# Kernel optimization log

Hardware: AMD Instinct MI355X
Metric: run time of the kernel (lower is better)

Reference implementation:

```python
import jax, jax.numpy as jnp
import numpy as np

DIM = 256
HEADS = 8
H = 56
W = 56
WS = 7          # window size
SHIFT = 3       # cyclic shift
MLP_HIDDEN = 4 * DIM
HEAD_DIM = DIM // HEADS
SCALE = HEAD_DIM ** -0.5
N = WS * WS     # tokens per window
EPS = 1e-5


def _rel_pos_index():
    coords = np.stack(np.meshgrid(np.arange(WS), np.arange(WS), indexing='ij'))  # [2,ws,ws]
    cf = coords.reshape(2, -1)                       # [2, N]
    rel = cf[:, :, None] - cf[:, None, :]            # [2, N, N]
    rel = rel.transpose(1, 2, 0).copy()              # [N, N, 2]
    rel[:, :, 0] += WS - 1
    rel[:, :, 1] += WS - 1
    rel[:, :, 1] *= 2 * WS - 1
    return rel.sum(-1)                               # [N, N]

REL_IDX = jnp.asarray(_rel_pos_index())


def _attn_mask():
    # shifted-window attention mask, computed once (static)
    img = np.zeros((H, W))
    cnt = 0
    slices = (slice(0, -WS), slice(-WS, -SHIFT), slice(-SHIFT, None))
    for hs in slices:
        for ws in slices:
            img[hs, ws] = cnt
            cnt += 1
    mw = img.reshape(H // WS, WS, W // WS, WS).transpose(0, 2, 1, 3).reshape(-1, N)  # [nW, N]
    am = mw[:, None, :] - mw[:, :, None]
    return jnp.asarray(np.where(am != 0, -100.0, 0.0).astype(np.float32))  # [nW, N, N]

ATTN_MASK = _attn_mask()


def _layernorm(y, g, b):
    mu = y.mean(-1, keepdims=True)
    var = ((y - mu) ** 2).mean(-1, keepdims=True)
    return (y - mu) * jax.lax.rsqrt(var + EPS) * g + b


def setup_inputs() -> dict:
    key = jax.random.key(0)
    ks = jax.random.split(key, 10)
    B = 32
    x = jax.random.normal(ks[0], (B, H * W, DIM), dtype=jnp.float32)
    qkv_w = jax.random.normal(ks[1], (DIM, 3 * DIM), dtype=jnp.float32) * 0.02
    qkv_b = jnp.zeros((3 * DIM,), dtype=jnp.float32)
    proj_w = jax.random.normal(ks[2], (DIM, DIM), dtype=jnp.float32) * 0.02
    proj_b = jnp.zeros((DIM,), dtype=jnp.float32)
    bias_table = jax.random.normal(ks[3], ((2 * WS - 1) * (2 * WS - 1), HEADS), dtype=jnp.float32) * 0.02
    norm1_g = jnp.ones((DIM,), dtype=jnp.float32)
    norm1_b = jnp.zeros((DIM,), dtype=jnp.float32)
    norm2_g = jnp.ones((DIM,), dtype=jnp.float32)
    norm2_b = jnp.zeros((DIM,), dtype=jnp.float32)
    mlp_w1 = jax.random.normal(ks[4], (DIM, MLP_HIDDEN), dtype=jnp.float32) * 0.02
    mlp_b1 = jnp.zeros((MLP_HIDDEN,), dtype=jnp.float32)
    mlp_w2 = jax.random.normal(ks[5], (MLP_HIDDEN, DIM), dtype=jnp.float32) * 0.02
    mlp_b2 = jnp.zeros((DIM,), dtype=jnp.float32)
    return dict(x=x, norm1_g=norm1_g, norm1_b=norm1_b, qkv_w=qkv_w, qkv_b=qkv_b,
                proj_w=proj_w, proj_b=proj_b, bias_table=bias_table,
                norm2_g=norm2_g, norm2_b=norm2_b,
                mlp_w1=mlp_w1, mlp_b1=mlp_b1, mlp_w2=mlp_w2, mlp_b2=mlp_b2)


def reference(x, norm1_g, norm1_b, qkv_w, qkv_b, proj_w, proj_b, bias_table,
              norm2_g, norm2_b, mlp_w1, mlp_b1, mlp_w2, mlp_b2):
    B, M, C = x.shape
    shortcut = x
    y = _layernorm(x, norm1_g, norm1_b).reshape(B, H, W, C)
    # cyclic shift
    y = jnp.roll(y, (-SHIFT, -SHIFT), axis=(1, 2))
    # window partition: [B,H,W,C] -> [B*nW, N, C]
    win = y.reshape(B, H // WS, WS, W // WS, WS, C).transpose(0, 1, 3, 2, 4, 5).reshape(-1, N, C)
    Bw = win.shape[0]
    qkv = (win @ qkv_w + qkv_b).reshape(Bw, N, 3, HEADS, HEAD_DIM).transpose(2, 0, 3, 1, 4)
    q, k, v = qkv[0], qkv[1], qkv[2]               # each [Bw, heads, N, hd]
    attn = jnp.einsum('bhnd,bhmd->bhnm', q, k) * SCALE
    bias = bias_table[REL_IDX].transpose(2, 0, 1)  # [heads, N, N]
    attn = attn + bias[None]
    nW = ATTN_MASK.shape[0]
    attn = attn.reshape(B, nW, HEADS, N, N) + ATTN_MASK[None, :, None]
    attn = jax.nn.softmax(attn.reshape(Bw, HEADS, N, N), axis=-1)
    out = jnp.einsum('bhnm,bhmd->bhnd', attn, v).transpose(0, 2, 1, 3).reshape(Bw, N, C)
    out = out @ proj_w + proj_b
    # window reverse and un-shift
    out = out.reshape(B, H // WS, W // WS, WS, WS, C).transpose(0, 1, 3, 2, 4, 5).reshape(B, H, W, C)
    out = jnp.roll(out, (SHIFT, SHIFT), axis=(1, 2)).reshape(B, M, C)
    x = shortcut + out
    h = _layernorm(x, norm2_g, norm2_b)
    h = jax.nn.gelu(h @ mlp_w1 + mlp_b1) @ mlp_w2 + mlp_b2
    return x + h
```

## Files before the change

### kernel.cpp

```cpp
#include <hip/hip_runtime.h>
#include <hip/hip_bf16.h>
#include <math.h>

typedef __bf16 bf16_t;
typedef __attribute__((ext_vector_type(8))) __bf16 bf16x8;
typedef __attribute__((ext_vector_type(4))) __bf16 bf16x4;
typedef __attribute__((ext_vector_type(4))) float f32x4;

#define T_TOK 100352
#define DIMC 256
#define HEADS 8
#define HD 32
#define NTOK 49
#define SHIFT3 3
#define HH 56
#define SCALE_QK 0.17677669529663687f

__device__ __forceinline__ int xrow_of(int rr) {
    int wi = rr / 49; int t = rr - wi * 49;
    int b = wi >> 6; int w64 = wi & 63;
    int wh = w64 >> 3, ww = w64 & 7;
    int i = t / 7, j = t - i * 7;
    int hy = wh * 7 + i, wy = ww * 7 + j;
    int hx = hy + SHIFT3; if (hx >= HH) hx -= HH;
    int wx = wy + SHIFT3; if (wx >= HH) wx -= HH;
    return b * (HH * HH) + hx * HH + wx;
}

__global__ __launch_bounds__(256) void transpose_cast(const float* __restrict__ W,
                                                      bf16_t* __restrict__ WT,
                                                      int K, int Nc) {
    int t = blockIdx.x * 256 + threadIdx.x;
    int k = t / Nc, c = t - k * Nc;
    WT[(size_t)c * K + k] = (bf16_t)W[t];
}

template <int MAP>
__global__ __launch_bounds__(256) void ln_kernel(const float* __restrict__ x,
                                                 const float* __restrict__ g,
                                                 const float* __restrict__ bsh,
                                                 bf16_t* __restrict__ out) {
    int wv = threadIdx.x >> 6, l = threadIdx.x & 63;
    int r = blockIdx.x * 4 + wv;
    int xr = MAP ? xrow_of(r) : r;
    float4 v = ((const float4*)(x + (size_t)xr * DIMC))[l];
    float s = v.x + v.y + v.z + v.w;
    float sq = v.x * v.x + v.y * v.y + v.z * v.z + v.w * v.w;
    #pragma unroll
    for (int off = 32; off; off >>= 1) {
        s += __shfl_down(s, off);
        sq += __shfl_down(sq, off);
    }
    s = __shfl(s, 0); sq = __shfl(sq, 0);
    float mean = s * (1.f / 256.f);
    float var = sq * (1.f / 256.f) - mean * mean;
    float rstd = rsqrtf(var + 1e-5f);
    float4 gv = ((const float4*)g)[l];
    float4 bv = ((const float4*)bsh)[l];
    bf16x4 o;
    o[0] = (bf16_t)((v.x - mean) * rstd * gv.x + bv.x);
    o[1] = (bf16_t)((v.y - mean) * rstd * gv.y + bv.y);
    o[2] = (bf16_t)((v.z - mean) * rstd * gv.z + bv.z);
    o[3] = (bf16_t)((v.w - mean) * rstd * gv.w + bv.w);
    *(bf16x4*)(out + (size_t)r * DIMC + l * 4) = o;
}

template <int EPI>
__global__ __launch_bounds__(256) void gemm128(const bf16_t* __restrict__ A,
                                               const bf16_t* __restrict__ BT,
                                               const float* __restrict__ bias,
                                               int Nc, int K,
                                               bf16_t* __restrict__ outb,
                                               float* __restrict__ outf,
                                               const float* __restrict__ resid) {
    __shared__ bf16_t As[128 * 32];
    __shared__ bf16_t Bs[128 * 32];
    int tid = threadIdx.x;
    int wv = tid >> 6, l = tid & 63;
    int wr = wv >> 1, wc = wv & 1;
    int nTilesN = Nc >> 7;
    int bm = blockIdx.x / nTilesN, bn = blockIdx.x - bm * nTilesN;
    size_t row0 = (size_t)bm * 128;
    int col0 = bn * 128;

    const char* Abase = (const char*)(A + row0 * K);
    const char* Bbase = (const char*)(BT + (size_t)col0 * K);
    const size_t ldb = (size_t)K * 2;

    f32x4 acc[4][4] = {};
    const int lr = l & 15, lk = (l >> 4) * 8;
    const int aoff = (wr * 64 + lr) * 32 + lk;
    const int boff = (wc * 64 + lr) * 32 + lk;

    for (int kk = 0; kk < K; kk += 32) {
        #pragma unroll
        for (int it = 0; it < 2; ++it) {
            int t = tid + it * 256;
            int row = t >> 2, cb = (t & 3) * 16;
            __builtin_amdgcn_global_load_lds(
                (const __attribute__((address_space(1))) void*)(Abase + (size_t)row * ldb + (size_t)kk * 2 + cb),
                (__attribute__((address_space(3))) void*)((char*)As + t * 16), 16, 0, 0);
            __builtin_amdgcn_global_load_lds(
                (const __attribute__((address_space(1))) void*)(Bbase + (size_t)row * ldb + (size_t)kk * 2 + cb),
                (__attribute__((address_space(3))) void*)((char*)Bs + t * 16), 16, 0, 0);
        }
        __syncthreads();
        bf16x8 a[4], b[4];
        #pragma unroll
        for (int m = 0; m < 4; ++m) a[m] = *(const bf16x8*)(As + aoff + m * 16 * 32);
        #pragma unroll
        for (int n = 0; n < 4; ++n) b[n] = *(const bf16x8*)(Bs + boff + n * 16 * 32);
        #pragma unroll
        for (int m = 0; m < 4; ++m)
            #pragma unroll
            for (int n = 0; n < 4; ++n)
                acc[m][n] = __builtin_amdgcn_mfma_f32_16x16x32_bf16(a[m], b[n], acc[m][n], 0, 0, 0);
        __syncthreads();
    }

    #pragma unroll
    for (int m = 0; m < 4; ++m) {
        #pragma unroll
        for (int i = 0; i < 4; ++i) {
            int rr = (int)row0 + wr * 64 + m * 16 + (l >> 4) * 4 + i;
            size_t orow = (EPI == 3) ? (size_t)xrow_of(rr) * DIMC : (size_t)rr * Nc;
            #pragma unroll
            for (int n = 0; n < 4; ++n) {
                int cc = col0 + wc * 64 + n * 16 + (l & 15);
                float v = acc[m][n][i] + bias[cc];
                if (EPI == 0) {
                    outb[(size_t)rr * Nc + cc] = (bf16_t)v;
                } else if (EPI == 1) {
                    float t = v + 0.044715f * v * v * v;
                    float gl = 0.5f * v * (1.f + tanhf(0.7978845608028654f * t));
                    outb[(size_t)rr * Nc + cc] = (bf16_t)gl;
                } else if (EPI == 2) {
                    size_t o = (size_t)rr * Nc + cc;
                    outf[o] = v + resid[o];
                } else {
                    size_t o = orow + cc;
                    outf[o] = v + resid[o];
                }
            }
        }
    }
}

__global__ __launch_bounds__(256) void attn_mfma(const bf16_t* __restrict__ qkv,
                                                 const float* __restrict__ bt,
                                                 bf16_t* __restrict__ out) {
    __shared__ __align__(16) char lds[4][12800];
    int wv = threadIdx.x >> 6, l = threadIdx.x & 63;
    int head = ((blockIdx.x & 1) << 2) | wv;
    int wi = blockIdx.x >> 1;
    char* W = lds[wv];
    bf16_t* Vt = (bf16_t*)(W + 8192);
    size_t rowbase = (size_t)wi * NTOK;
    const bf16_t* src = qkv + rowbase * 768 + head * HD;

    int w64 = wi & 63;
    int wh = w64 >> 3, ww = w64 & 7;
    bool lastH = (wh == 7), lastW = (ww == 7);
    bool masked = lastH || lastW;

    #pragma unroll
    for (int it = 0; it < 4; ++it) {
        int t = l + it * 64;
        int r = t >> 2, g = t & 3;
        if (r < NTOK) {
            bf16x8 qv = *(const bf16x8*)(src + (size_t)r * 768 + g * 8);
            bf16x8 kv = *(const bf16x8*)(src + (size_t)r * 768 + 256 + g * 8);
            int sa = (r * 64 + g * 16) ^ ((r & 7) << 4);
            *(bf16x8*)(W + sa) = qv;
            *(bf16x8*)(W + 4096 + sa) = kv;
        }
    }
    #pragma unroll
    for (int it = 0; it < 4; ++it) {
        int t = l + it * 64;
        int m = t >> 2, dc = t & 3;
        if (m < NTOK) {
            bf16x8 vv = *(const bf16x8*)(src + (size_t)m * 768 + 512 + dc * 8);
            #pragma unroll
            for (int j = 0; j < 8; ++j) Vt[(dc * 8 + j) * 72 + m] = vv[j];
        } else {
            #pragma unroll
            for (int j = 0; j < 8; ++j) Vt[(dc * 8 + j) * 72 + m] = (bf16_t)0.f;
        }
    }

    int lr = l & 15, g4 = l >> 4;

    bf16x8 a[4], b[4];
    #pragma unroll
    for (int mt = 0; mt < 4; ++mt) {
        int r = mt * 16 + lr;
        int sa = (r * 64 + g4 * 16) ^ ((r & 7) << 4);
        a[mt] = *(const bf16x8*)(W + sa);
        b[mt] = *(const bf16x8*)(W + 4096 + sa);
    }
    f32x4 z = {0.f, 0.f, 0.f, 0.f};
    f32x4 S[4][4];
    #pragma unroll
    for (int mt = 0; mt < 4; ++mt)
        #pragma unroll
        for (int nt = 0; nt < 4; ++nt)
            S[mt][nt] = __builtin_amdgcn_mfma_f32_16x16x32_bf16(a[mt], b[nt], z, 0, 0, 0);

    int i2[4], j2[4], reg2[4];
    #pragma unroll
    for (int nt = 0; nt < 4; ++nt) {
        int cm = nt * 16 + lr;
        i2[nt] = (cm * 147) >> 10;
        j2[nt] = cm - i2[nt] * 7;
        int rh = lastH ? ((i2[nt] < 4) ? 1 : 2) : 0;
        int rw = lastW ? ((j2[nt] < 4) ? 1 : 2) : 0;
        reg2[nt] = rh * 3 + rw;
    }

    #pragma unroll
    for (int mt = 0; mt < 4; ++mt) {
        #pragma unroll
        for (int i = 0; i < 4; ++i) {
            int rn = mt * 16 + g4 * 4 + i;
            bool rowok = rn < NTOK;
            int i1 = (rn * 147) >> 10, j1 = rn - i1 * 7;
            int rh1 = lastH ? ((i1 < 4) ? 1 : 2) : 0;
            int rw1 = lastW ? ((j1 < 4) ? 1 : 2) : 0;
            int reg1 = rh1 * 3 + rw1;
            float sv[4];
            #pragma unroll
            for (int nt = 0; nt < 4; ++nt) {
                int cm = nt * 16 + lr;
                float s;
                if (rowok && cm < NTOK) {
                    s = S[mt][nt][i] * SCALE_QK;
                    s += bt[((i1 - i2[nt] + 6) + 13 * (j1 - j2[nt] + 6)) * 8 + head];
                    if (masked && (reg1 != reg2[nt])) s -= 100.f;
                } else {
                    s = -1e30f;
                }
                sv[nt] = s;
            }
            float mx = fmaxf(fmaxf(sv[0], sv[1]), fmaxf(sv[2], sv[3]));
            mx = fmaxf(mx, __shfl_xor(mx, 1));
            mx = fmaxf(mx, __shfl_xor(mx, 2));
            mx = fmaxf(mx, __shfl_xor(mx, 4));
            mx = fmaxf(mx, __shfl_xor(mx, 8));
            float e[4];
            float sum = 0.f;
            #pragma unroll
            for (int nt = 0; nt < 4; ++nt) { e[nt] = __expf(sv[nt] - mx); sum += e[nt]; }
            sum += __shfl_xor(sum, 1);
            sum += __shfl_xor(sum, 2);
            sum += __shfl_xor(sum, 4);
            sum += __shfl_xor(sum, 8);
            float inv = 1.f / sum;
            #pragma unroll
            for (int nt = 0; nt < 4; ++nt) {
                int cm = nt * 16 + lr;
                int pa = (rn * 128 + cm * 2) ^ ((rn & 7) << 4);
                *(bf16_t*)(W + pa) = (bf16_t)(e[nt] * inv);
            }
        }
    }

    f32x4 o[4][2] = {};
    #pragma unroll
    for (int ks = 0; ks < 2; ++ks) {
        bf16x8 pa[4], vb[2];
        #pragma unroll
        for (int mt = 0; mt < 4; ++mt) {
            int r = mt * 16 + lr;
            int ad = (r * 128 + ks * 64 + g4 * 16) ^ ((r & 7) << 4);
            pa[mt] = *(const bf16x8*)(W + ad);
        }
        #pragma unroll
        for (int dt = 0; dt < 2; ++dt) {
            int d = dt * 16 + lr;
            vb[dt] = *(const bf16x8*)((char*)Vt + d * 144 + ks * 64 + g4 * 16);
        }
        #pragma unroll
        for (int mt = 0; mt < 4; ++mt)
            #pragma unroll
            for (int dt = 0; dt < 2; ++dt)
                o[mt][dt] = __builtin_amdgcn_mfma_f32_16x16x32_bf16(pa[mt], vb[dt], o[mt][dt], 0, 0, 0);
    }

    #pragma unroll
    for (int mt = 0; mt < 4; ++mt) {
        #pragma unroll
        for (int i = 0; i < 4; ++i) {
            int n = mt * 16 + g4 * 4 + i;
            if (n < NTOK) {
                #pragma unroll
                for (int dt = 0; dt < 2; ++dt) {
                    out[(rowbase + n) * DIMC + head * HD + dt * 16 + lr] = (bf16_t)o[mt][dt][i];
                }
            }
        }
    }
}

extern "C" void kernel_launch(void* const* d_in, const int* in_sizes, int n_in,
                              void* d_out, int out_size, void* d_ws, size_t ws_size,
                              hipStream_t stream) {
    const float* x      = (const float*)d_in[0];
    const float* n1g    = (const float*)d_in[1];
    const float* n1b    = (const float*)d_in[2];
    const float* qkv_w  = (const float*)d_in[3];
    const float* qkv_b  = (const float*)d_in[4];
    const float* proj_w = (const float*)d_in[5];
    const float* proj_b = (const float*)d_in[6];
    const float* btab   = (const float*)d_in[7];
    const float* n2g    = (const float*)d_in[8];
    const float* n2b    = (const float*)d_in[9];
    const float* w1     = (const float*)d_in[10];
    const float* b1     = (const float*)d_in[11];
    const float* w2     = (const float*)d_in[12];
    const float* b2     = (const float*)d_in[13];

    char* ws = (char*)d_ws;
    bf16_t* win      = (bf16_t*)(ws);
    bf16_t* qkvbuf   = (bf16_t*)(ws + (size_t)T_TOK * 256 * 2);
    bf16_t* mlp1_buf = (bf16_t*)(ws);
    bf16_t* h2       = (bf16_t*)(ws + (size_t)T_TOK * 2048);
    char* wtp        = ws + (size_t)T_TOK * 2048 + (size_t)T_TOK * 512;
    bf16_t* wt_qkv   = (bf16_t*)wtp;
    bf16_t* wt_proj  = wt_qkv + 768 * 256;
    bf16_t* wt_mlp1  = wt_proj + 256 * 256;
    bf16_t* wt_mlp2  = wt_mlp1 + 1024 * 256;
    float* xmid      = (float*)d_out;

    transpose_cast<<<768, 256, 0, stream>>>(qkv_w, wt_qkv, 256, 768);
    transpose_cast<<<256, 256, 0, stream>>>(proj_w, wt_proj, 256, 256);
    transpose_cast<<<1024, 256, 0, stream>>>(w1, wt_mlp1, 256, 1024);
    transpose_cast<<<1024, 256, 0, stream>>>(w2, wt_mlp2, 1024, 256);

    ln_kernel<1><<<T_TOK / 4, 256, 0, stream>>>(x, n1g, n1b, win);
    gemm128<0><<<(T_TOK / 128) * (768 / 128), 256, 0, stream>>>(win, wt_qkv, qkv_b, 768, 256,
                                                                qkvbuf, nullptr, nullptr);
    attn_mfma<<<2048 * 2, 256, 0, stream>>>(qkvbuf, btab, win);
    gemm128<3><<<(T_TOK / 128) * (256 / 128), 256, 0, stream>>>(win, wt_proj, proj_b, 256, 256,
                                                                nullptr, xmid, x);
    ln_kernel<0><<<T_TOK / 4, 256, 0, stream>>>(xmid, n2g, n2b, h2);
    gemm128<1><<<(T_TOK / 128) * (1024 / 128), 256, 0, stream>>>(h2, wt_mlp1, b1, 1024, 256,
                                                                 mlp1_buf, nullptr, nullptr);
    gemm128<2><<<(T_TOK / 128) * (256 / 128), 256, 0, stream>>>(mlp1_buf, wt_mlp2, b2, 256, 1024,
                                                                nullptr, xmid, xmid);
}
```

Baseline: 599.6 us.

## Fuse LayerNorm2, MLP fc1+GELU and fc2 into one kernel; remap GEMM blocks

Replaces the second LayerNorm, the fc1 GEMM with GELU epilogue and the fc2 GEMM with one kernel. Each 64-row block normalises its rows in registers, streams 128-column slices of W1 into LDS, writes the GELU output to swizzled LDS, and accumulates fc2 directly. This removes the round trips of the 1024-wide hidden activation and the normalised input through HBM. GELU now uses an exp/rcp sigmoid form instead of tanhf, and block indices are remapped in strides of 8 (likely aimed at XCD placement). The price is 80KB of LDS per block, which limits occupancy, and weights are reloaded per block with no overlap between loads and MFMA.

```diff
diff --git a/kernel.cpp b/kernel.cpp
--- a/kernel.cpp
+++ b/kernel.cpp
@@ -79,7 +79,9 @@
     int wv = tid >> 6, l = tid & 63;
     int wr = wv >> 1, wc = wv & 1;
     int nTilesN = Nc >> 7;
-    int bm = blockIdx.x / nTilesN, bn = blockIdx.x - bm * nTilesN;
+    int qn = gridDim.x >> 3;
+    int lb = (blockIdx.x & 7) * qn + (blockIdx.x >> 3);
+    int bm = lb / nTilesN, bn = lb - bm * nTilesN;
     size_t row0 = (size_t)bm * 128;
     int col0 = bn * 128;
 
@@ -130,10 +132,6 @@
                 float v = acc[m][n][i] + bias[cc];
                 if (EPI == 0) {
                     outb[(size_t)rr * Nc + cc] = (bf16_t)v;
-                } else if (EPI == 1) {
-                    float t = v + 0.044715f * v * v * v;
-                    float gl = 0.5f * v * (1.f + tanhf(0.7978845608028654f * t));
-                    outb[(size_t)rr * Nc + cc] = (bf16_t)gl;
                 } else if (EPI == 2) {
                     size_t o = (size_t)rr * Nc + cc;
                     outf[o] = v + resid[o];
@@ -142,6 +140,129 @@
                     outf[o] = v + resid[o];
                 }
             }
+        }
+    }
+}
+
+__global__ __launch_bounds__(256) void mlp_fused(const float* __restrict__ xio,
+                                                 const float* __restrict__ g2,
+                                                 const float* __restrict__ bsh2,
+                                                 const bf16_t* __restrict__ w1t,
+                                                 const float* __restrict__ bias1,
+                                                 const bf16_t* __restrict__ w2t,
+                                                 const float* __restrict__ bias2,
+                                                 float* __restrict__ outx) {
+    __shared__ __align__(16) char Wsl[65536];
+    __shared__ __align__(16) char hq[16384];
+    int tid = threadIdx.x, wv = tid >> 6, l = tid & 63;
+    int g4 = l >> 4, lr = l & 15;
+    int qn = gridDim.x >> 3;
+    int lb = (blockIdx.x & 7) * qn + (blockIdx.x >> 3);
+    size_t rows0 = (size_t)lb * 64;
+    int myrow = (int)rows0 + wv * 16 + lr;
+
+    const float* xr = xio + (size_t)myrow * 256;
+    float xv[8][8];
+    float s = 0.f, sq = 0.f;
+    #pragma unroll
+    for (int f = 0; f < 8; ++f) {
+        float4 u0 = *(const float4*)(xr + f * 32 + g4 * 8);
+        float4 u1 = *(const float4*)(xr + f * 32 + g4 * 8 + 4);
+        xv[f][0] = u0.x; xv[f][1] = u0.y; xv[f][2] = u0.z; xv[f][3] = u0.w;
+        xv[f][4] = u1.x; xv[f][5] = u1.y; xv[f][6] = u1.z; xv[f][7] = u1.w;
+        s  += u0.x + u0.y + u0.z + u0.w + u1.x + u1.y + u1.z + u1.w;
+        sq += u0.x*u0.x + u0.y*u0.y + u0.z*u0.z + u0.w*u0.w
+            + u1.x*u1.x + u1.y*u1.y + u1.z*u1.z + u1.w*u1.w;
+    }
+    s  += __shfl_xor(s, 16);  s  += __shfl_xor(s, 32);
+    sq += __shfl_xor(sq, 16); sq += __shfl_xor(sq, 32);
+    float mean = s * (1.f / 256.f);
+    float rstd = rsqrtf(sq * (1.f / 256.f) - mean * mean + 1e-5f);
+    bf16x8 a[8];
+    #pragma unroll
+    for (int f = 0; f < 8; ++f) {
+        float4 gv0 = *(const float4*)(g2 + f * 32 + g4 * 8);
+        float4 gv1 = *(const float4*)(g2 + f * 32 + g4 * 8 + 4);
+        float4 bv0 = *(const float4*)(bsh2 + f * 32 + g4 * 8);
+        float4 bv1 = *(const float4*)(bsh2 + f * 32 + g4 * 8 + 4);
+        float gg[8] = {gv0.x, gv0.y, gv0.z, gv0.w, gv1.x, gv1.y, gv1.z, gv1.w};
+        float bb[8] = {bv0.x, bv0.y, bv0.z, bv0.w, bv1.x, bv1.y, bv1.z, bv1.w};
+        #pragma unroll
+        for (int j = 0; j < 8; ++j)
+            a[f][j] = (bf16_t)((xv[f][j] - mean) * rstd * gg[j] + bb[j]);
+    }
+
+    f32x4 acc[16] = {};
+    char* HB = hq + wv * 4096;
+
+    for (int p = 0; p < 8; ++p) {
+        __syncthreads();
+        #pragma unroll
+        for (int it = 0; it < 16; ++it) {
+            int t = tid + it * 256;
+            int c = t >> 5, kc = (t & 31) ^ (c & 7);
+            __builtin_amdgcn_global_load_lds(
+                (const __attribute__((address_space(1))) void*)((const char*)w1t + ((size_t)(p * 128 + c) * 256 + kc * 8) * 2),
+                (__attribute__((address_space(3))) void*)(Wsl + t * 16), 16, 0, 0);
+        }
+        __syncthreads();
+        f32x4 c1[8] = {};
+        #pragma unroll
+        for (int ks = 0; ks < 8; ++ks) {
+            #pragma unroll
+            for (int n = 0; n < 8; ++n) {
+                int c = n * 16 + lr;
+                int byte = (c * 512 + ks * 64 + g4 * 16) ^ ((c & 7) << 4);
+                bf16x8 b = *(const bf16x8*)(Wsl + byte);
+                c1[n] = __builtin_amdgcn_mfma_f32_16x16x32_bf16(a[ks], b, c1[n], 0, 0, 0);
+            }
+        }
+        #pragma unroll
+        for (int n = 0; n < 8; ++n) {
+            float b1v = bias1[p * 128 + n * 16 + lr];
+            #pragma unroll
+            for (int i = 0; i < 4; ++i) {
+                int r4 = g4 * 4 + i;
+                float v = c1[n][i] + b1v;
+                float t3 = v + 0.044715f * v * v * v;
+                float e = __expf(-1.5957691216057308f * t3);
+                float gl = v * __builtin_amdgcn_rcpf(1.f + e);
+                int byte = (r4 * 256 + (n * 16 + lr) * 2) ^ ((r4 & 7) << 4);
+                *(bf16_t*)(HB + byte) = (bf16_t)gl;
+            }
+        }
+        __syncthreads();
+        #pragma unroll
+        for (int it = 0; it < 16; ++it) {
+            int t = tid + it * 256;
+            int c = t >> 4, kc = (t & 15) ^ (c & 7);
+            __builtin_amdgcn_global_load_lds(
+                (const __attribute__((address_space(1))) void*)((const char*)w2t + ((size_t)c * 1024 + p * 128 + kc * 8) * 2),
+                (__attribute__((address_space(3))) void*)(Wsl + t * 16), 16, 0, 0);
+        }
+        __syncthreads();
+        #pragma unroll
+        for (int ks = 0; ks < 4; ++ks) {
+            int abyte = (lr * 256 + ks * 64 + g4 * 16) ^ ((lr & 7) << 4);
+            bf16x8 a2 = *(const bf16x8*)(HB + abyte);
+            #pragma unroll
+            for (int n = 0; n < 16; ++n) {
+                int c = n * 16 + lr;
+                int byte = (c * 256 + ks * 64 + g4 * 16) ^ ((c & 7) << 4);
+                bf16x8 b = *(const bf16x8*)(Wsl + byte);
+                acc[n] = __builtin_amdgcn_mfma_f32_16x16x32_bf16(a2, b, acc[n], 0, 0, 0);
+            }
+        }
+    }
+
+    #pragma unroll
+    for (int n = 0; n < 16; ++n) {
+        int cc = n * 16 + lr;
+        float b2v = bias2[cc];
+        #pragma unroll
+        for (int i = 0; i < 4; ++i) {
+            size_t o = (rows0 + wv * 16 + g4 * 4 + i) * 256 + cc;
+            outx[o] = acc[n][i] + b2v + xio[o];
         }
     }
 }
@@ -232,15 +353,15 @@
             #pragma unroll
             for (int nt = 0; nt < 4; ++nt) {
                 int cm = nt * 16 + lr;
-                float s;
+                float sc;
                 if (rowok && cm < NTOK) {
-                    s = S[mt][nt][i] * SCALE_QK;
-                    s += bt[((i1 - i2[nt] + 6) + 13 * (j1 - j2[nt] + 6)) * 8 + head];
-                    if (masked && (reg1 != reg2[nt])) s -= 100.f;
+                    sc = S[mt][nt][i] * SCALE_QK;
+                    sc += bt[((i1 - i2[nt] + 6) + 13 * (j1 - j2[nt] + 6)) * 8 + head];
+                    if (masked && (reg1 != reg2[nt])) sc -= 100.f;
                 } else {
-                    s = -1e30f;
+                    sc = -1e30f;
                 }
-                sv[nt] = s;
+                sv[nt] = sc;
             }
             float mx = fmaxf(fmaxf(sv[0], sv[1]), fmaxf(sv[2], sv[3]));
             mx = fmaxf(mx, __shfl_xor(mx, 1));
@@ -323,8 +444,6 @@
     char* ws = (char*)d_ws;
     bf16_t* win      = (bf16_t*)(ws);
     bf16_t* qkvbuf   = (bf16_t*)(ws + (size_t)T_TOK * 256 * 2);
-    bf16_t* mlp1_buf = (bf16_t*)(ws);
-    bf16_t* h2       = (bf16_t*)(ws + (size_t)T_TOK * 2048);
     char* wtp        = ws + (size_t)T_TOK * 2048 + (size_t)T_TOK * 512;
     bf16_t* wt_qkv   = (bf16_t*)wtp;
     bf16_t* wt_proj  = wt_qkv + 768 * 256;
@@ -343,9 +462,5 @@
     attn_mfma<<<2048 * 2, 256, 0, stream>>>(qkvbuf, btab, win);
     gemm128<3><<<(T_TOK / 128) * (256 / 128), 256, 0, stream>>>(win, wt_proj, proj_b, 256, 256,
                                                                 nullptr, xmid, x);
-    ln_kernel<0><<<T_TOK / 4, 256, 0, stream>>>(xmid, n2g, n2b, h2);
-    gemm128<1><<<(T_TOK / 128) * (1024 / 128), 256, 0, stream>>>(h2, wt_mlp1, b1, 1024, 256,
-                                                                 mlp1_buf, nullptr, nullptr);
-    gemm128<2><<<(T_TOK / 128) * (256 / 128), 256, 0, stream>>>(mlp1_buf, wt_mlp2, b2, 256, 1024,
-                                                                nullptr, xmid, xmid);
-}
+    mlp_fused<<<T_TOK / 64, 256, 0, stream>>>(xmid, n2g, n2b, wt_mlp1, b1, wt_mlp2, b2, xmid);
+}
```

Result: slower. 756.4 us (+26.2%).
